# Optimization experiments

Hardware: AMD Instinct MI355X
Metric: run time of the kernel (lower is better)

Reference implementation:

```python
import jax, jax.numpy as jnp
import numpy as np

N, D_IN, D_OUT = 2048, 128, 64


def setup_inputs() -> dict:
    key = jax.random.key(0)
    k1, k2, k3, k4 = jax.random.split(key, 4)
    node_features = jax.random.normal(k1, (N, D_IN), dtype=jnp.float32)
    neighbor_mask = jax.random.randint(k2, (N, N), 0, 2) > 0
    W = jax.random.normal(k3, (D_OUT, D_IN), dtype=jnp.float32) * (1.0 / np.sqrt(D_IN))
    a = jax.random.normal(k4, (2 * D_OUT,), dtype=jnp.float32)
    return {"node_features": node_features, "neighbor_mask": neighbor_mask, "W": W, "a": a}


def reference(node_features, neighbor_mask, W, a):
    # h = Linear(node_features): [N, D_OUT]
    h = node_features @ W.T
    d = h.shape[-1]
    # Additive-attention decomposition: einsum('ijn,n->ij', cat[h_i,h_j], a)
    # == (h @ a[:d])_i + (h @ a[d:])_j  -- same math, no NxNx2D tensor.
    s_i = h @ a[:d]  # [N]
    s_j = h @ a[d:]  # [N]
    scores = jax.nn.leaky_relu(s_i[:, None] + s_j[None, :], negative_slope=0.01)  # [N, N]
    neg_inf = jnp.array(-jnp.inf, dtype=scores.dtype)
    scores = jnp.where(neighbor_mask, scores, neg_inf)
    valid = jnp.any(neighbor_mask, axis=1, keepdims=True)  # [N, 1]
    scores = jnp.where(valid, scores, 0.0)
    alpha = jax.nn.softmax(scores, axis=1)
    alpha = jnp.where(neighbor_mask, alpha, 0.0)
    # messages[i, j, :] = alpha[i, j] * h[j]
    messages = alpha[:, :, None] * h[None, :, :]  # [N, N, D_OUT]
    return messages
```

## Files before the change

kernel.cpp:

```cpp
#include <hip/hip_runtime.h>
#include <math.h>

#define GN 2048
#define GD_IN 128
#define GD_OUT 64

typedef float f4 __attribute__((ext_vector_type(4)));

__global__ __launch_bounds__(64) void gat_h_kernel(
    const float* __restrict__ x,
    const float* __restrict__ W,
    const float* __restrict__ a,
    float* __restrict__ h,
    float* __restrict__ s_i,
    float* __restrict__ s_j) {
    __shared__ float wl[GD_OUT * (GD_IN + 1)];
    __shared__ float xl[GD_IN];
    const int i = blockIdx.x;
    const int t = threadIdx.x;

    for (int idx = t; idx < GD_OUT * GD_IN; idx += 64) {
        int o = idx >> 7, k = idx & 127;
        wl[o * (GD_IN + 1) + k] = W[idx];
    }
    xl[t]      = x[i * GD_IN + t];
    xl[t + 64] = x[i * GD_IN + t + 64];
    __syncthreads();

    float acc = 0.f;
    const float* wr = &wl[t * (GD_IN + 1)];
    #pragma unroll
    for (int k = 0; k < GD_IN; ++k) acc = fmaf(xl[k], wr[k], acc);
    h[i * GD_OUT + t] = acc;

    float p1 = acc * a[t];
    float p2 = acc * a[GD_OUT + t];
    #pragma unroll
    for (int off = 32; off; off >>= 1) {
        p1 += __shfl_down(p1, off);
        p2 += __shfl_down(p2, off);
    }
    if (t == 0) { s_i[i] = p1; s_j[i] = p2; }
}

__global__ __launch_bounds__(256) void gat_msg_kernel(
    const int* __restrict__ mask,
    const float* __restrict__ h,
    const float* __restrict__ s_i,
    const float* __restrict__ s_j,
    float* __restrict__ out) {
    __shared__ float sc[GN];
    __shared__ float red[8];
    const int i = blockIdx.x;
    const int t = threadIdx.x;
    const float si = s_i[i];

    float lmax = -INFINITY;
    for (int j = t; j < GN; j += 256) {
        float z = si + s_j[j];
        float s = z > 0.f ? z : 0.01f * z;
        int m = mask[(size_t)i * GN + j];
        s = m ? s : -INFINITY;
        sc[j] = s;
        lmax = fmaxf(lmax, s);
    }
    #pragma unroll
    for (int off = 32; off; off >>= 1) lmax = fmaxf(lmax, __shfl_down(lmax, off));
    if ((t & 63) == 0) red[t >> 6] = lmax;
    __syncthreads();
    float rmax = fmaxf(fmaxf(red[0], red[1]), fmaxf(red[2], red[3]));
    if (rmax == -INFINITY) rmax = 0.f;

    float lsum = 0.f;
    for (int j = t; j < GN; j += 256) {
        float e = expf(sc[j] - rmax);
        sc[j] = e;
        lsum += e;
    }
    #pragma unroll
    for (int off = 32; off; off >>= 1) lsum += __shfl_down(lsum, off);
    __syncthreads();
    if ((t & 63) == 0) red[t >> 6] = lsum;
    __syncthreads();
    float ssum = red[0] + red[1] + red[2] + red[3];
    const float inv = ssum > 0.f ? 1.f / ssum : 0.f;

    const f4* __restrict__ h4 = reinterpret_cast<const f4*>(h);
    f4* __restrict__ out4 = reinterpret_cast<f4*>(out) + (size_t)i * GN * (GD_OUT / 4);
    const int jl = t >> 4;
    const int o4 = t & 15;
    #pragma unroll 4
    for (int jb = 0; jb < GN; jb += 16) {
        int j = jb + jl;
        float al = sc[j] * inv;
        f4 hv = h4[j * (GD_OUT / 4) + o4];
        f4 r = hv * al;
        __builtin_nontemporal_store(r, &out4[(size_t)j * (GD_OUT / 4) + o4]);
    }
}

extern "C" void kernel_launch(void* const* d_in, const int* in_sizes, int n_in,
                              void* d_out, int out_size, void* d_ws, size_t ws_size,
                              hipStream_t stream) {
    const float* x    = (const float*)d_in[0];
    const int*   mask = (const int*)d_in[1];
    const float* W    = (const float*)d_in[2];
    const float* a    = (const float*)d_in[3];
    float* out = (float*)d_out;

    float* ws  = (float*)d_ws;
    float* h   = ws;
    float* s_i = ws + GN * GD_OUT;
    float* s_j = s_i + GN;

    gat_h_kernel<<<GN, 64, 0, stream>>>(x, W, a, h, s_i, s_j);
    gat_msg_kernel<<<GN, 256, 0, stream>>>(mask, h, s_i, s_j, out);
}
```

Before: 222.6 us.

## Split softmax row stats from output write into separate grid-strided kernels

The fused per-row message kernel is split in two. One kernel computes each row's max and inverse sum and stores them with s_i in a small per-row record. A second flat kernel recomputes each alpha from s_i, s_j and the mask, then streams the 1 GB output, with each thread holding one fixed h[j] vector across rows. The aim is a more uniform store stream with h kept in registers and no shared-memory dependency. In exchange it adds a kernel launch, reads the mask twice, recomputes the exponentials, and switches to the fast __expf.

New measurement: 256.6 us. +15.3%, slower.

```diff
diff --git a/kernel.cpp b/kernel.cpp
--- a/kernel.cpp
+++ b/kernel.cpp
@@ -43,14 +43,13 @@
     if (t == 0) { s_i[i] = p1; s_j[i] = p2; }
 }
 
-__global__ __launch_bounds__(256) void gat_msg_kernel(
+__global__ __launch_bounds__(256) void gat_rowstat_kernel(
     const int* __restrict__ mask,
-    const float* __restrict__ h,
     const float* __restrict__ s_i,
     const float* __restrict__ s_j,
-    float* __restrict__ out) {
+    f4* __restrict__ rowp) {
     __shared__ float sc[GN];
-    __shared__ float red[8];
+    __shared__ float red[4];
     const int i = blockIdx.x;
     const int t = threadIdx.x;
     const float si = s_i[i];
@@ -59,8 +58,7 @@
     for (int j = t; j < GN; j += 256) {
         float z = si + s_j[j];
         float s = z > 0.f ? z : 0.01f * z;
-        int m = mask[(size_t)i * GN + j];
-        s = m ? s : -INFINITY;
+        s = mask[(size_t)i * GN + j] ? s : -INFINITY;
         sc[j] = s;
         lmax = fmaxf(lmax, s);
     }
@@ -72,30 +70,46 @@
     if (rmax == -INFINITY) rmax = 0.f;
 
     float lsum = 0.f;
-    for (int j = t; j < GN; j += 256) {
-        float e = expf(sc[j] - rmax);
-        sc[j] = e;
-        lsum += e;
-    }
+    for (int j = t; j < GN; j += 256) lsum += __expf(sc[j] - rmax);
     #pragma unroll
     for (int off = 32; off; off >>= 1) lsum += __shfl_down(lsum, off);
     __syncthreads();
     if ((t & 63) == 0) red[t >> 6] = lsum;
     __syncthreads();
-    float ssum = red[0] + red[1] + red[2] + red[3];
-    const float inv = ssum > 0.f ? 1.f / ssum : 0.f;
+    if (t == 0) {
+        float ssum = red[0] + red[1] + red[2] + red[3];
+        f4 rp;
+        rp.x = si;
+        rp.y = rmax;
+        rp.z = ssum > 0.f ? 1.f / ssum : 0.f;
+        rp.w = 0.f;
+        rowp[i] = rp;
+    }
+}
 
-    const f4* __restrict__ h4 = reinterpret_cast<const f4*>(h);
-    f4* __restrict__ out4 = reinterpret_cast<f4*>(out) + (size_t)i * GN * (GD_OUT / 4);
-    const int jl = t >> 4;
+__global__ __launch_bounds__(256) void gat_write_kernel(
+    const int* __restrict__ mask,
+    const float* __restrict__ h,
+    const float* __restrict__ s_j,
+    const f4* __restrict__ rowp,
+    f4* __restrict__ out4) {
+    const int t = blockIdx.x * 256 + threadIdx.x;
     const int o4 = t & 15;
+    const int j  = (t >> 4) & (GN - 1);
+    const f4 hv = reinterpret_cast<const f4*>(h)[(j << 4) | o4];
+    const float sj = s_j[j];
+
+    size_t f = (size_t)t;
     #pragma unroll 4
-    for (int jb = 0; jb < GN; jb += 16) {
-        int j = jb + jl;
-        float al = sc[j] * inv;
-        f4 hv = h4[j * (GD_OUT / 4) + o4];
-        f4 r = hv * al;
-        __builtin_nontemporal_store(r, &out4[(size_t)j * (GD_OUT / 4) + o4]);
+    for (int it = 0; it < (GN * GN * 16) / (2048 * 256); ++it, f += 2048 * 256) {
+        const int i = (int)(f >> 15);
+        const f4 rp = rowp[i];
+        const int m = mask[f >> 4];
+        float z = rp.x + sj;
+        float s = z > 0.f ? z : 0.01f * z;
+        float e = __expf(s - rp.y) * rp.z;
+        float al = m ? e : 0.f;
+        __builtin_nontemporal_store(hv * al, &out4[f]);
     }
 }
 
@@ -112,7 +126,9 @@
     float* h   = ws;
     float* s_i = ws + GN * GD_OUT;
     float* s_j = s_i + GN;
+    f4*    rowp = (f4*)(s_j + GN);
 
     gat_h_kernel<<<GN, 64, 0, stream>>>(x, W, a, h, s_i, s_j);
-    gat_msg_kernel<<<GN, 256, 0, stream>>>(mask, h, s_i, s_j, out);
+    gat_rowstat_kernel<<<GN, 256, 0, stream>>>(mask, s_i, s_j, rowp);
+    gat_write_kernel<<<2048, 256, 0, stream>>>(mask, h, s_j, rowp, (f4*)out);
 }
```
